# Kernel optimization log

Measured on AMD Instinct MI355X. Metric: run time of the kernel, lower is better.

The kernel has to match this reference:

```python
import jax, jax.numpy as jnp
import numpy as np

D_MODEL = 1024
NUM_HEADS = 16
D_HEAD = D_MODEL // NUM_HEADS


def setup_inputs() -> dict:
    key = jax.random.key(0)
    ks = jax.random.split(key, 9)
    s = 1.0 / np.sqrt(D_MODEL)
    return {
        "x": jax.random.normal(ks[0], (2, 2048, D_MODEL), dtype=jnp.float32),
        "Wq": jax.random.normal(ks[1], (D_MODEL, D_MODEL), dtype=jnp.float32) * s,
        "bq": jnp.zeros((D_MODEL,), dtype=jnp.float32),
        "Wk": jax.random.normal(ks[2], (D_MODEL, D_MODEL), dtype=jnp.float32) * s,
        "bk": jnp.zeros((D_MODEL,), dtype=jnp.float32),
        "Wv": jax.random.normal(ks[3], (D_MODEL, D_MODEL), dtype=jnp.float32) * s,
        "bv": jnp.zeros((D_MODEL,), dtype=jnp.float32),
        "Wo": jax.random.normal(ks[4], (D_MODEL, D_MODEL), dtype=jnp.float32) * s,
        "bo": jnp.zeros((D_MODEL,), dtype=jnp.float32),
    }


def reference(x, Wq, bq, Wk, bk, Wv, bv, Wo, bo):
    B, S, D = x.shape
    H, Dh = NUM_HEADS, D_HEAD

    def split_heads(t):  # [B,S,D] -> [B,H,S,Dh]
        return t.reshape(B, S, H, Dh).transpose(0, 2, 1, 3)

    # Linear layers: y = x @ W^T + b (torch nn.Linear convention)
    Q = split_heads(x @ Wq.T + bq)
    K = split_heads(x @ Wk.T + bk)
    V = split_heads(x @ Wv.T + bv)

    scale = 1.0 / jnp.sqrt(jnp.asarray(Dh, dtype=x.dtype))
    scores = jnp.einsum("bhqd,bhkd->bhqk", Q, K) * scale  # [B,H,S,S]
    attn = jax.nn.softmax(scores, axis=-1)
    context = jnp.einsum("bhqk,bhkd->bhqd", attn, V)  # [B,H,S,Dh]
    context = context.transpose(0, 2, 1, 3).reshape(B, S, D)
    return context @ Wo.T + bo
```

## Files before the change

### kernel.cpp

```cpp
#include <hip/hip_runtime.h>


#define T_TOK 4096
#define DM    1024
#define SQ    2048
#define NH    16
#define DH    64

typedef unsigned short u16;
typedef unsigned int   u32;
typedef __bf16 bf16x8 __attribute__((ext_vector_type(8)));
typedef float  f32x4  __attribute__((ext_vector_type(4)));
typedef float  f32x16 __attribute__((ext_vector_type(16)));
typedef u32    u32x4  __attribute__((ext_vector_type(4)));

__device__ __forceinline__ u16 f2bf(float f) {
  u32 u = __builtin_bit_cast(u32, f);
  u32 r = (u + 0x7FFFu + ((u >> 16) & 1u)) >> 16;
  return (u16)r;
}

#if __has_builtin(__builtin_amdgcn_cvt_pk_bf16_f32)
typedef __bf16 bf16x2 __attribute__((ext_vector_type(2)));
__device__ __forceinline__ u32 pk2bf(float a, float b) {
  bf16x2 h = __builtin_amdgcn_cvt_pk_bf16_f32(a, b);
  return __builtin_bit_cast(u32, h);
}
#else
__device__ __forceinline__ u32 pk2bf(float a, float b) {
  u32 r;
  asm("v_cvt_pk_bf16_f32 %0, %1, %2" : "=v"(r) : "v"(a), "v"(b));
  return r;
}
#endif

__device__ __forceinline__ void gld16(const void* g, void* l) {
  __builtin_amdgcn_global_load_lds(
      (const __attribute__((address_space(1))) u32*)g,
      (__attribute__((address_space(3))) u32*)l, 16, 0, 0);
}

__global__ void cast_bf16_kernel(const float* __restrict__ x,
    const float* __restrict__ w0, const float* __restrict__ w1,
    const float* __restrict__ w2, const float* __restrict__ w3,
    u16* __restrict__ xb, u16* __restrict__ o0, u16* __restrict__ o1,
    u16* __restrict__ o2, u16* __restrict__ o3)
{
  const float* src; u16* dst; int n;
  switch (blockIdx.y) {
    case 0:  src = x;  dst = xb; n = T_TOK * DM; break;
    case 1:  src = w0; dst = o0; n = DM * DM; break;
    case 2:  src = w1; dst = o1; n = DM * DM; break;
    case 3:  src = w2; dst = o2; n = DM * DM; break;
    default: src = w3; dst = o3; n = DM * DM; break;
  }
  const int stride = gridDim.x * blockDim.x;
  for (int i = blockIdx.x * blockDim.x + threadIdx.x; i * 4 < n; i += stride) {
    float4 v = ((const float4*)src)[i];
    ushort4 o;
    o.x = f2bf(v.x); o.y = f2bf(v.y); o.z = f2bf(v.z); o.w = f2bf(v.w);
    ((ushort4*)dst)[i] = o;
  }
}

__device__ __forceinline__ void gemm_core_128x128(
    u16* lds, const u16* __restrict__ Ab, const u16* __restrict__ Bb,
    f32x4 acc[4][4])
{
  u16* As = lds;
  u16* Bs = lds + 8192;
  const int tid = threadIdx.x, lane = tid & 63, w = tid >> 6;
  const int waveM = w >> 1, waveN = w & 1;
  const int col = lane & 15, quad = lane >> 4;
  const int srow = lane >> 3;
  const int sg0  = (lane & 7) ^ srow;

  for (int k0 = 0; k0 < DM; k0 += 64) {
    #pragma unroll
    for (int i = 0; i < 4; ++i) {
      const int rb = w * 32 + i * 8;
      const int sg = sg0 ^ ((rb >> 3) & 3);
      gld16(Ab + (size_t)(rb + srow) * DM + k0 + sg * 8, &As[rb * 64]);
      gld16(Bb + (size_t)(rb + srow) * DM + k0 + sg * 8, &Bs[rb * 64]);
    }
    __syncthreads();
    #pragma unroll
    for (int c = 0; c < 2; ++c) {
      bf16x8 af[4], bg[4];
      #pragma unroll
      for (int i = 0; i < 4; ++i) {
        const int row = waveM * 64 + i * 16 + col;
        const int gp = (c * 4 + quad) ^ (row & 7) ^ ((row >> 3) & 3);
        af[i] = *(const bf16x8*)&As[row * 64 + gp * 8];
      }
      #pragma unroll
      for (int j = 0; j < 4; ++j) {
        const int row = waveN * 64 + j * 16 + col;
        const int gp = (c * 4 + quad) ^ (row & 7) ^ ((row >> 3) & 3);
        bg[j] = *(const bf16x8*)&Bs[row * 64 + gp * 8];
      }
      #pragma unroll
      for (int i = 0; i < 4; ++i) {
        #pragma unroll
        for (int j = 0; j < 4; ++j)
          acc[i][j] = __builtin_amdgcn_mfma_f32_16x16x32_bf16(af[i], bg[j], acc[i][j], 0, 0, 0);
      }
    }
    __syncthreads();
  }
}

__device__ __forceinline__ void gemm_core_128x64(
    u16* lds, const u16* __restrict__ Ab, const u16* __restrict__ Bb,
    f32x4 acc[4][2])
{
  u16* As = lds;
  u16* Bs = lds + 8192;
  const int tid = threadIdx.x, lane = tid & 63, w = tid >> 6;
  const int waveM = w >> 1, waveN = w & 1;
  const int col = lane & 15, quad = lane >> 4;
  const int srow = lane >> 3;
  const int sg0  = (lane & 7) ^ srow;

  for (int k0 = 0; k0 < DM; k0 += 64) {
    #pragma unroll
    for (int i = 0; i < 4; ++i) {
      const int rb = w * 32 + i * 8;
      const int sg = sg0 ^ ((rb >> 3) & 3);
      gld16(Ab + (size_t)(rb + srow) * DM + k0 + sg * 8, &As[rb * 64]);
    }
    #pragma unroll
    for (int i = 0; i < 2; ++i) {
      const int rb = w * 16 + i * 8;
      const int sg = sg0 ^ ((rb >> 3) & 3);
      gld16(Bb + (size_t)(rb + srow) * DM + k0 + sg * 8, &Bs[rb * 64]);
    }
    __syncthreads();
    #pragma unroll
    for (int c = 0; c < 2; ++c) {
      bf16x8 af[4], bg[2];
      #pragma unroll
      for (int i = 0; i < 4; ++i) {
        const int row = waveM * 64 + i * 16 + col;
        const int gp = (c * 4 + quad) ^ (row & 7) ^ ((row >> 3) & 3);
        af[i] = *(const bf16x8*)&As[row * 64 + gp * 8];
      }
      #pragma unroll
      for (int j = 0; j < 2; ++j) {
        const int row = waveN * 32 + j * 16 + col;
        const int gp = (c * 4 + quad) ^ (row & 7) ^ ((row >> 3) & 3);
        bg[j] = *(const bf16x8*)&Bs[row * 64 + gp * 8];
      }
      #pragma unroll
      for (int i = 0; i < 4; ++i) {
        #pragma unroll
        for (int j = 0; j < 2; ++j)
          acc[i][j] = __builtin_amdgcn_mfma_f32_16x16x32_bf16(af[i], bg[j], acc[i][j], 0, 0, 0);
      }
    }
    __syncthreads();
  }
}

__global__ __launch_bounds__(256) void gemm_qkv_kernel(
    const u16* __restrict__ xb,
    const u16* __restrict__ Wqb, const u16* __restrict__ Wkb, const u16* __restrict__ Wvb,
    const float* __restrict__ bq, const float* __restrict__ bk, const float* __restrict__ bv,
    u16* __restrict__ Qs, u16* __restrict__ Kh, u16* __restrict__ Vt)
{
  __shared__ __align__(16) u16 smem[128 * 136];
  u16* tr = smem;
  const int z = blockIdx.z;
  const u16*   Wb   = (z == 0) ? Wqb : (z == 1) ? Wkb : Wvb;
  const float* bias = (z == 0) ? bq  : (z == 1) ? bk  : bv;
  const float scale = (z == 0) ? 0.18033688011112042f : 1.0f;

  const int tid = threadIdx.x;
  const int lane = tid & 63, w = tid >> 6;
  const int waveM = w >> 1, waveN = w & 1;
  const int col = lane & 15, quad = lane >> 4;
  const f32x4 zf = {0.f, 0.f, 0.f, 0.f};

  if (z == 2) {
    if (blockIdx.y >= 32) return;
    f32x4 acc[4][4];
    #pragma unroll
    for (int i = 0; i < 4; ++i) {
      #pragma unroll
      for (int j = 0; j < 4; ++j) acc[i][j] = zf;
    }
    gemm_core_128x128(smem, xb + (size_t)(blockIdx.y * 128) * DM,
                      Wb + (size_t)(blockIdx.x * 128) * DM, acc);
    #pragma unroll
    for (int j = 0; j < 4; ++j) {
      const int cl = waveN * 64 + j * 16 + col;
      const float bb = bias[blockIdx.x * 128 + cl];
      #pragma unroll
      for (int i = 0; i < 4; ++i) {
        const int tl = waveM * 64 + i * 16 + quad * 4;
        ushort4 pk;
        pk.x = f2bf(acc[i][j][0] + bb); pk.y = f2bf(acc[i][j][1] + bb);
        pk.z = f2bf(acc[i][j][2] + bb); pk.w = f2bf(acc[i][j][3] + bb);
        *(ushort4*)&tr[cl * 136 + tl] = pk;
      }
    }
    __syncthreads();
    const int t0 = blockIdx.y * 128;
    const int b = t0 >> 11, sBase = t0 & 2047;
    #pragma unroll
    for (int rep = 0; rep < 8; ++rep) {
      const int chunk = rep * 256 + tid;
      const int row = chunk >> 4, off = (chunk & 15) * 8;
      const int c = blockIdx.x * 128 + row;
      const int h = c >> 6, d = c & 63;
      uint4 v = *(const uint4*)&tr[row * 136 + off];
      *(uint4*)&Vt[((size_t)(b * NH + h) * DH + d) * SQ + sBase + off] = v;
    }
  } else {
    f32x4 acc[4][2];
    #pragma unroll
    for (int i = 0; i < 4; ++i) {
      #pragma unroll
      for (int j = 0; j < 2; ++j) acc[i][j] = zf;
    }
    gemm_core_128x64(smem, Wb + (size_t)(blockIdx.x * 128) * DM,
                     xb + (size_t)(blockIdx.y * 64) * DM, acc);
    u16* out = (z == 0) ? Qs : Kh;
    const int chBase  = blockIdx.x * 128 + waveM * 64;
    const int tokBase = blockIdx.y * 64 + waveN * 32;
    #pragma unroll
    for (int i = 0; i < 4; ++i) {
      const int c0 = chBase + i * 16 + quad * 4;
      const int hh = c0 >> 6, d0 = c0 & 63;
      const float4 bb = *(const float4*)&bias[c0];
      #pragma unroll
      for (int j = 0; j < 2; ++j) {
        const int t = tokBase + j * 16 + col;
        const int b = t >> 11, s = t & 2047;
        ushort4 pk;
        pk.x = f2bf((acc[i][j][0] + bb.x) * scale);
        pk.y = f2bf((acc[i][j][1] + bb.y) * scale);
        pk.z = f2bf((acc[i][j][2] + bb.z) * scale);
        pk.w = f2bf((acc[i][j][3] + bb.w) * scale);
        *(ushort4*)&out[((size_t)(b * NH + hh) * SQ + s) * DH + d0] = pk;
      }
    }
  }
}

__global__ __launch_bounds__(256, 2) void attn_kernel(
    const u16* __restrict__ Qs, const u16* __restrict__ Kh,
    const u16* __restrict__ Vt, u16* __restrict__ ctx)
{
  __shared__ __align__(16) char smem[64 * 1024];
  u16* KtB = (u16*)smem;
  u16* VlB = (u16*)(smem + 32768);
  f32x4* red  = (f32x4*)smem;
  float* lred = (float*)(smem + 32768);

  const int tid = threadIdx.x, lane = tid & 63, w = tid >> 6;
  const int l31 = lane & 31, h = lane >> 5;
  const int bh = blockIdx.y, q0 = blockIdx.x * 64;
  const u16* Qb = Qs + ((size_t)bh * SQ + q0) * DH;
  const u16* Kb = Kh + (size_t)bh * SQ * DH;
  const u16* Vb = Vt + (size_t)bh * DH * SQ;

  bf16x8 qreg[2][4];
  #pragma unroll
  for (int qt = 0; qt < 2; ++qt) {
    #pragma unroll
    for (int ks = 0; ks < 4; ++ks)
      qreg[qt][ks] = *(const bf16x8*)(Qb + (size_t)(qt * 32 + l31) * DH
                                         + ks * 16 + h * 8);
  }

  #pragma unroll
  for (int i = 0; i < 4; ++i) {
    const int rb = w * 32 + i * 8;
    const int rowloc = rb + (lane >> 3);
    const int sg = (lane & 7) ^ (lane >> 3) ^ ((rb >> 3) & 3);
    gld16(Kb + (size_t)rowloc * DH + sg * 8, &KtB[rb * 64]);
  }
  #pragma unroll
  for (int i = 0; i < 4; ++i) {
    const int rb = w * 16 + i * 4;
    const int rowloc = rb + (lane >> 4);
    const int sg = (lane & 15) ^ (rowloc & 15);
    gld16(Vb + (size_t)rowloc * SQ + sg * 8, &VlB[rb * 128]);
  }

  f32x16 cacc[2][2];
  #pragma unroll
  for (int dt = 0; dt < 2; ++dt)
    #pragma unroll
    for (int qt = 0; qt < 2; ++qt)
      #pragma unroll
      for (int e = 0; e < 16; ++e) cacc[dt][qt][e] = 0.f;
  float l_s[2] = {0.f, 0.f};
  __syncthreads();

  for (int kt = 0; kt < SQ / 128; ++kt) {
    const int cur = kt & 1;
    u16* Kt = KtB + cur * 8192;
    u16* Vl = VlB + cur * 8192;
    if (kt + 1 < SQ / 128) {
      const int nxt = cur ^ 1, s1 = (kt + 1) * 128;
      u16* Ktn = KtB + nxt * 8192;
      u16* Vln = VlB + nxt * 8192;
      #pragma unroll
      for (int i = 0; i < 4; ++i) {
        const int rb = w * 32 + i * 8;
        const int rowloc = rb + (lane >> 3);
        const int sg = (lane & 7) ^ (lane >> 3) ^ ((rb >> 3) & 3);
        gld16(Kb + (size_t)(s1 + rowloc) * DH + sg * 8, &Ktn[rb * 64]);
      }
      #pragma unroll
      for (int i = 0; i < 4; ++i) {
        const int rb = w * 16 + i * 4;
        const int rowloc = rb + (lane >> 4);
        const int sg = (lane & 15) ^ (rowloc & 15);
        gld16(Vb + (size_t)rowloc * SQ + s1 + sg * 8, &Vln[rb * 128]);
      }
    }

    f32x16 sacc[2];
    #pragma unroll
    for (int qt = 0; qt < 2; ++qt)
      #pragma unroll
      for (int e = 0; e < 16; ++e) sacc[qt][e] = 0.f;
    #pragma unroll
    for (int ks = 0; ks < 4; ++ks) {
      const int row = w * 32 + l31;
      const int gp = (2 * ks + h) ^ (l31 & 7) ^ ((l31 >> 3) & 3);
      bf16x8 kf = *(const bf16x8*)&Kt[row * 64 + gp * 8];
      sacc[0] = __builtin_amdgcn_mfma_f32_32x32x16_bf16(kf, qreg[0][ks], sacc[0], 0, 0, 0);
      sacc[1] = __builtin_amdgcn_mfma_f32_32x32x16_bf16(kf, qreg[1][ks], sacc[1], 0, 0, 0);
    }

    u32 Pp[2][4][2];
    #pragma unroll
    for (int qt = 0; qt < 2; ++qt) {
      float p[16];
      #pragma unroll
      for (int e = 0; e < 16; ++e)
        p[e] = __builtin_amdgcn_exp2f(sacc[qt][e]);
      float t0 = (p[0] + p[1]) + (p[2] + p[3]);
      float t1 = (p[4] + p[5]) + (p[6] + p[7]);
      float t2 = (p[8] + p[9]) + (p[10] + p[11]);
      float t3 = (p[12] + p[13]) + (p[14] + p[15]);
      l_s[qt] += (t0 + t1) + (t2 + t3);
      #pragma unroll
      for (int rg = 0; rg < 4; ++rg) {
        Pp[qt][rg][0] = pk2bf(p[4 * rg + 0], p[4 * rg + 1]);
        Pp[qt][rg][1] = pk2bf(p[4 * rg + 2], p[4 * rg + 3]);
      }
    }

    #pragma unroll
    for (int ks = 0; ks < 2; ++ks) {
      bf16x8 pf[2];
      #pragma unroll
      for (int qt = 0; qt < 2; ++qt) {
        u32 own0 = h ? Pp[qt][2 * ks + 1][0] : Pp[qt][2 * ks][0];
        u32 own1 = h ? Pp[qt][2 * ks + 1][1] : Pp[qt][2 * ks][1];
        u32 snd0 = h ? Pp[qt][2 * ks][0] : Pp[qt][2 * ks + 1][0];
        u32 snd1 = h ? Pp[qt][2 * ks][1] : Pp[qt][2 * ks + 1][1];
        u32 rcv0 = (u32)__shfl_xor((int)snd0, 32, 64);
        u32 rcv1 = (u32)__shfl_xor((int)snd1, 32, 64);
        u32x4 fw;
        fw.x = h ? rcv0 : own0;
        fw.y = h ? rcv1 : own1;
        fw.z = h ? own0 : rcv0;
        fw.w = h ? own1 : rcv1;
        pf[qt] = __builtin_bit_cast(bf16x8, fw);
      }
      #pragma unroll
      for (int dt = 0; dt < 2; ++dt) {
        const int row = dt * 32 + l31;
        const int gp = (4 * w + 2 * ks + h) ^ (row & 15);
        bf16x8 vf = *(const bf16x8*)&Vl[row * 128 + gp * 8];
        cacc[dt][0] = __builtin_amdgcn_mfma_f32_32x32x16_bf16(vf, pf[0], cacc[dt][0], 0, 0, 0);
        cacc[dt][1] = __builtin_amdgcn_mfma_f32_32x32x16_bf16(vf, pf[1], cacc[dt][1], 0, 0, 0);
      }
    }
    __syncthreads();
  }

  float lq[2];
  #pragma unroll
  for (int qt = 0; qt < 2; ++qt) {
    lq[qt] = l_s[qt] + __shfl_xor(l_s[qt], 32, 64);
    if (h == 0) lred[(w * 2 + qt) * 32 + l31] = lq[qt];
  }
  const int b = bh >> 4, hd = bh & 15;
  #pragma unroll
  for (int qt = 0; qt < 2; ++qt) {
    __syncthreads();
    #pragma unroll
    for (int dt = 0; dt < 2; ++dt) {
      #pragma unroll
      for (int c = 0; c < 4; ++c) {
        f32x4 ch;
        ch[0] = cacc[dt][qt][4 * c + 0]; ch[1] = cacc[dt][qt][4 * c + 1];
        ch[2] = cacc[dt][qt][4 * c + 2]; ch[3] = cacc[dt][qt][4 * c + 3];
        red[((w * 2 + dt) * 4 + c) * 64 + lane] = ch;
      }
    }
    __syncthreads();
    const int dt = w >> 1, c0 = (w & 1) * 2;
    f32x4 sum[2];
    #pragma unroll
    for (int j = 0; j < 2; ++j) { sum[j][0]=0; sum[j][1]=0; sum[j][2]=0; sum[j][3]=0; }
    #pragma unroll
    for (int sw = 0; sw < 4; ++sw) {
      #pragma unroll
      for (int j = 0; j < 2; ++j)
        sum[j] += red[((sw * 2 + dt) * 4 + c0 + j) * 64 + lane];
    }
    float lsum = lred[(0 * 2 + qt) * 32 + l31] + lred[(1 * 2 + qt) * 32 + l31]
               + lred[(2 * 2 + qt) * 32 + l31] + lred[(3 * 2 + qt) * 32 + l31];
    const float inv = 1.0f / lsum;
    const int s = q0 + qt * 32 + l31;
    #pragma unroll
    for (int j = 0; j < 2; ++j) {
      const int d0 = dt * 32 + (c0 + j) * 8 + 4 * h;
      ushort4 pk;
      pk.x = f2bf(sum[j][0] * inv); pk.y = f2bf(sum[j][1] * inv);
      pk.z = f2bf(sum[j][2] * inv); pk.w = f2bf(sum[j][3] * inv);
      *(ushort4*)&ctx[(size_t)(b * SQ + s) * DM + hd * DH + d0] = pk;
    }
  }
}

__global__ __launch_bounds__(256) void gemm_out_kernel(
    const u16* __restrict__ ctx, const u16* __restrict__ Wob,
    const float* __restrict__ bo, float* __restrict__ out)
{
  __shared__ __align__(16) u16 As[64 * 64];
  __shared__ __align__(16) u16 Bs[64 * 64];
  const u16* Ab = ctx + (size_t)(blockIdx.y * 64) * DM;
  const u16* Bb = Wob + (size_t)(blockIdx.x * 64) * DM;
  const int tid = threadIdx.x, lane = tid & 63, w = tid >> 6;
  const int waveM = w >> 1, waveN = w & 1;
  const int col = lane & 15, quad = lane >> 4;
  const int srow = lane >> 3;
  const int sg0  = (lane & 7) ^ srow;

  f32x4 acc[2][2];
  const f32x4 zf = {0.f, 0.f, 0.f, 0.f};
  #pragma unroll
  for (int i = 0; i < 2; ++i) {
    #pragma unroll
    for (int j = 0; j < 2; ++j) acc[i][j] = zf;
  }

  for (int k0 = 0; k0 < DM; k0 += 64) {
    #pragma unroll
    for (int i = 0; i < 2; ++i) {
      const int rb = w * 16 + i * 8;
      const int sg = sg0 ^ ((rb >> 3) & 3);
      gld16(Ab + (size_t)(rb + srow) * DM + k0 + sg * 8, &As[rb * 64]);
      gld16(Bb + (size_t)(rb + srow) * DM + k0 + sg * 8, &Bs[rb * 64]);
    }
    __syncthreads();
    #pragma unroll
    for (int c = 0; c < 2; ++c) {
      bf16x8 af[2], bg[2];
      #pragma unroll
      for (int i = 0; i < 2; ++i) {
        const int row = waveM * 32 + i * 16 + col;
        const int gp = (c * 4 + quad) ^ (row & 7) ^ ((row >> 3) & 3);
        af[i] = *(const bf16x8*)&As[row * 64 + gp * 8];
      }
      #pragma unroll
      for (int j = 0; j < 2; ++j) {
        const int row = waveN * 32 + j * 16 + col;
        const int gp = (c * 4 + quad) ^ (row & 7) ^ ((row >> 3) & 3);
        bg[j] = *(const bf16x8*)&Bs[row * 64 + gp * 8];
      }
      #pragma unroll
      for (int i = 0; i < 2; ++i) {
        #pragma unroll
        for (int j = 0; j < 2; ++j)
          acc[i][j] = __builtin_amdgcn_mfma_f32_16x16x32_bf16(af[i], bg[j], acc[i][j], 0, 0, 0);
      }
    }
    __syncthreads();
  }

  const int rowBase = blockIdx.y * 64 + waveM * 32;
  const int colBase = blockIdx.x * 64 + waveN * 32;
  #pragma unroll
  for (int j = 0; j < 2; ++j) {
    const int c = colBase + j * 16 + col;
    const float bb = bo[c];
    #pragma unroll
    for (int i = 0; i < 2; ++i) {
      #pragma unroll
      for (int r = 0; r < 4; ++r) {
        const int t = rowBase + i * 16 + quad * 4 + r;
        out[(size_t)t * DM + c] = acc[i][j][r] + bb;
      }
    }
  }
}

extern "C" void kernel_launch(void* const* d_in, const int* in_sizes, int n_in,
                              void* d_out, int out_size, void* d_ws, size_t ws_size,
                              hipStream_t stream) {
  const float* x  = (const float*)d_in[0];
  const float* Wq = (const float*)d_in[1];
  const float* bq = (const float*)d_in[2];
  const float* Wk = (const float*)d_in[3];
  const float* bk = (const float*)d_in[4];
  const float* Wv = (const float*)d_in[5];
  const float* bv = (const float*)d_in[6];
  const float* Wo = (const float*)d_in[7];
  const float* bo = (const float*)d_in[8];

  char* ws = (char*)d_ws;
  u16* xb  = (u16*)(ws);
  u16* Wqb = (u16*)(ws + (8ull  << 20));
  u16* Wkb = (u16*)(ws + (10ull << 20));
  u16* Wvb = (u16*)(ws + (12ull << 20));
  u16* Wob = (u16*)(ws + (14ull << 20));
  u16* Qs  = (u16*)(ws + (16ull << 20));
  u16* Kh  = (u16*)(ws + (24ull << 20));
  u16* Vt  = (u16*)(ws + (32ull << 20));
  u16* ctx = xb;

  cast_bf16_kernel<<<dim3(256, 5), 256, 0, stream>>>(x, Wq, Wk, Wv, Wo,
                                                     xb, Wqb, Wkb, Wvb, Wob);
  gemm_qkv_kernel<<<dim3(8, 64, 3), 256, 0, stream>>>(xb, Wqb, Wkb, Wvb,
                                                      bq, bk, bv, Qs, Kh, Vt);
  attn_kernel<<<dim3(32, 32), 256, 0, stream>>>(Qs, Kh, Vt, ctx);
  gemm_out_kernel<<<dim3(16, 64), 256, 0, stream>>>(ctx, Wob, bo, (float*)d_out);
  (void)in_sizes; (void)n_in; (void)out_size; (void)ws_size;
}
```

Before: 207.6 us.

## Shrink attention KV tile to 64 and split waves by query/key halves

The attention kernel now streams 64-key tiles instead of 128-key tiles. Each wave owns one 32-query tile and one 32-key sub-tile rather than two query tiles, which halves the accumulator and score registers per wave. LDS drops from 64KB to 33KB and launch bounds rise to 4 blocks per CU, aiming for higher occupancy and better latency hiding. The cost is twice as many loop iterations and barriers, and a different cross-wave reduction layout at the end.

```diff
diff --git a/kernel.cpp b/kernel.cpp
--- a/kernel.cpp
+++ b/kernel.cpp
@@ -248,187 +248,145 @@
   }
 }
 
-__global__ __launch_bounds__(256, 2) void attn_kernel(
+__global__ __launch_bounds__(256, 4) void attn_kernel(
     const u16* __restrict__ Qs, const u16* __restrict__ Kh,
     const u16* __restrict__ Vt, u16* __restrict__ ctx)
 {
-  __shared__ __align__(16) char smem[64 * 1024];
+  __shared__ __align__(16) char smem[33 * 1024];
   u16* KtB = (u16*)smem;
-  u16* VlB = (u16*)(smem + 32768);
+  u16* VlB = (u16*)(smem + 16384);
   f32x4* red  = (f32x4*)smem;
   float* lred = (float*)(smem + 32768);
 
   const int tid = threadIdx.x, lane = tid & 63, w = tid >> 6;
   const int l31 = lane & 31, h = lane >> 5;
+  const int qt = w & 1, st = w >> 1;
   const int bh = blockIdx.y, q0 = blockIdx.x * 64;
   const u16* Qb = Qs + ((size_t)bh * SQ + q0) * DH;
   const u16* Kb = Kh + (size_t)bh * SQ * DH;
   const u16* Vb = Vt + (size_t)bh * DH * SQ;
-
-  bf16x8 qreg[2][4];
-  #pragma unroll
-  for (int qt = 0; qt < 2; ++qt) {
-    #pragma unroll
-    for (int ks = 0; ks < 4; ++ks)
-      qreg[qt][ks] = *(const bf16x8*)(Qb + (size_t)(qt * 32 + l31) * DH
-                                         + ks * 16 + h * 8);
-  }
-
-  #pragma unroll
-  for (int i = 0; i < 4; ++i) {
-    const int rb = w * 32 + i * 8;
-    const int rowloc = rb + (lane >> 3);
-    const int sg = (lane & 7) ^ (lane >> 3) ^ ((rb >> 3) & 3);
-    gld16(Kb + (size_t)rowloc * DH + sg * 8, &KtB[rb * 64]);
-  }
-  #pragma unroll
-  for (int i = 0; i < 4; ++i) {
-    const int rb = w * 16 + i * 4;
-    const int rowloc = rb + (lane >> 4);
-    const int sg = (lane & 15) ^ (rowloc & 15);
-    gld16(Vb + (size_t)rowloc * SQ + sg * 8, &VlB[rb * 128]);
-  }
-
-  f32x16 cacc[2][2];
+  const int srow = lane >> 3;
+  const int sgl  = (lane & 7) ^ srow;
+
+  bf16x8 qreg[4];
+  #pragma unroll
+  for (int ks = 0; ks < 4; ++ks)
+    qreg[ks] = *(const bf16x8*)(Qb + (size_t)(qt * 32 + l31) * DH + ks * 16 + h * 8);
+
+  #pragma unroll
+  for (int i = 0; i < 2; ++i) {
+    const int rb = w * 16 + i * 8;
+    const int sg = sgl ^ ((rb >> 3) & 3);
+    gld16(Kb + (size_t)(rb + srow) * DH + sg * 8, &KtB[rb * 64]);
+    gld16(Vb + (size_t)(rb + srow) * SQ + sg * 8, &VlB[rb * 64]);
+  }
+
+  f32x16 cacc[2];
   #pragma unroll
   for (int dt = 0; dt < 2; ++dt)
     #pragma unroll
-    for (int qt = 0; qt < 2; ++qt)
-      #pragma unroll
-      for (int e = 0; e < 16; ++e) cacc[dt][qt][e] = 0.f;
-  float l_s[2] = {0.f, 0.f};
+    for (int e = 0; e < 16; ++e) cacc[dt][e] = 0.f;
+  float l_s = 0.f;
   __syncthreads();
 
-  for (int kt = 0; kt < SQ / 128; ++kt) {
+  for (int kt = 0; kt < SQ / 64; ++kt) {
     const int cur = kt & 1;
-    u16* Kt = KtB + cur * 8192;
-    u16* Vl = VlB + cur * 8192;
-    if (kt + 1 < SQ / 128) {
-      const int nxt = cur ^ 1, s1 = (kt + 1) * 128;
-      u16* Ktn = KtB + nxt * 8192;
-      u16* Vln = VlB + nxt * 8192;
-      #pragma unroll
-      for (int i = 0; i < 4; ++i) {
-        const int rb = w * 32 + i * 8;
-        const int rowloc = rb + (lane >> 3);
-        const int sg = (lane & 7) ^ (lane >> 3) ^ ((rb >> 3) & 3);
-        gld16(Kb + (size_t)(s1 + rowloc) * DH + sg * 8, &Ktn[rb * 64]);
-      }
-      #pragma unroll
-      for (int i = 0; i < 4; ++i) {
-        const int rb = w * 16 + i * 4;
-        const int rowloc = rb + (lane >> 4);
-        const int sg = (lane & 15) ^ (rowloc & 15);
-        gld16(Vb + (size_t)rowloc * SQ + s1 + sg * 8, &Vln[rb * 128]);
-      }
-    }
-
-    f32x16 sacc[2];
-    #pragma unroll
-    for (int qt = 0; qt < 2; ++qt)
-      #pragma unroll
-      for (int e = 0; e < 16; ++e) sacc[qt][e] = 0.f;
+    u16* Kt = KtB + cur * 4096;
+    u16* Vl = VlB + cur * 4096;
+    if (kt + 1 < SQ / 64) {
+      const int nxt = cur ^ 1, s1 = (kt + 1) * 64;
+      u16* Ktn = KtB + nxt * 4096;
+      u16* Vln = VlB + nxt * 4096;
+      #pragma unroll
+      for (int i = 0; i < 2; ++i) {
+        const int rb = w * 16 + i * 8;
+        const int sg = sgl ^ ((rb >> 3) & 3);
+        gld16(Kb + (size_t)(s1 + rb + srow) * DH + sg * 8, &Ktn[rb * 64]);
+        gld16(Vb + (size_t)(rb + srow) * SQ + s1 + sg * 8, &Vln[rb * 64]);
+      }
+    }
+
+    f32x16 sacc;
+    #pragma unroll
+    for (int e = 0; e < 16; ++e) sacc[e] = 0.f;
     #pragma unroll
     for (int ks = 0; ks < 4; ++ks) {
-      const int row = w * 32 + l31;
+      const int row = st * 32 + l31;
       const int gp = (2 * ks + h) ^ (l31 & 7) ^ ((l31 >> 3) & 3);
       bf16x8 kf = *(const bf16x8*)&Kt[row * 64 + gp * 8];
-      sacc[0] = __builtin_amdgcn_mfma_f32_32x32x16_bf16(kf, qreg[0][ks], sacc[0], 0, 0, 0);
-      sacc[1] = __builtin_amdgcn_mfma_f32_32x32x16_bf16(kf, qreg[1][ks], sacc[1], 0, 0, 0);
-    }
-
-    u32 Pp[2][4][2];
-    #pragma unroll
-    for (int qt = 0; qt < 2; ++qt) {
+      sacc = __builtin_amdgcn_mfma_f32_32x32x16_bf16(kf, qreg[ks], sacc, 0, 0, 0);
+    }
+
+    u32 Pp[4][2];
+    {
       float p[16];
       #pragma unroll
       for (int e = 0; e < 16; ++e)
-        p[e] = __builtin_amdgcn_exp2f(sacc[qt][e]);
+        p[e] = __builtin_amdgcn_exp2f(sacc[e]);
       float t0 = (p[0] + p[1]) + (p[2] + p[3]);
       float t1 = (p[4] + p[5]) + (p[6] + p[7]);
       float t2 = (p[8] + p[9]) + (p[10] + p[11]);
       float t3 = (p[12] + p[13]) + (p[14] + p[15]);
-      l_s[qt] += (t0 + t1) + (t2 + t3);
+      l_s += (t0 + t1) + (t2 + t3);
       #pragma unroll
       for (int rg = 0; rg < 4; ++rg) {
-        Pp[qt][rg][0] = pk2bf(p[4 * rg + 0], p[4 * rg + 1]);
-        Pp[qt][rg][1] = pk2bf(p[4 * rg + 2], p[4 * rg + 3]);
+        Pp[rg][0] = pk2bf(p[4 * rg + 0], p[4 * rg + 1]);
+        Pp[rg][1] = pk2bf(p[4 * rg + 2], p[4 * rg + 3]);
       }
     }
 
     #pragma unroll
     for (int ks = 0; ks < 2; ++ks) {
-      bf16x8 pf[2];
-      #pragma unroll
-      for (int qt = 0; qt < 2; ++qt) {
-        u32 own0 = h ? Pp[qt][2 * ks + 1][0] : Pp[qt][2 * ks][0];
-        u32 own1 = h ? Pp[qt][2 * ks + 1][1] : Pp[qt][2 * ks][1];
-        u32 snd0 = h ? Pp[qt][2 * ks][0] : Pp[qt][2 * ks + 1][0];
-        u32 snd1 = h ? Pp[qt][2 * ks][1] : Pp[qt][2 * ks + 1][1];
-        u32 rcv0 = (u32)__shfl_xor((int)snd0, 32, 64);
-        u32 rcv1 = (u32)__shfl_xor((int)snd1, 32, 64);
-        u32x4 fw;
-        fw.x = h ? rcv0 : own0;
-        fw.y = h ? rcv1 : own1;
-        fw.z = h ? own0 : rcv0;
-        fw.w = h ? own1 : rcv1;
-        pf[qt] = __builtin_bit_cast(bf16x8, fw);
-      }
+      u32 own0 = h ? Pp[2 * ks + 1][0] : Pp[2 * ks][0];
+      u32 own1 = h ? Pp[2 * ks + 1][1] : Pp[2 * ks][1];
+      u32 snd0 = h ? Pp[2 * ks][0] : Pp[2 * ks + 1][0];
+      u32 snd1 = h ? Pp[2 * ks][1] : Pp[2 * ks + 1][1];
+      u32 rcv0 = (u32)__shfl_xor((int)snd0, 32, 64);
+      u32 rcv1 = (u32)__shfl_xor((int)snd1, 32, 64);
+      u32x4 fw;
+      fw.x = h ? rcv0 : own0;
+      fw.y = h ? rcv1 : own1;
+      fw.z = h ? own0 : rcv0;
+      fw.w = h ? own1 : rcv1;
+      bf16x8 pf = __builtin_bit_cast(bf16x8, fw);
       #pragma unroll
       for (int dt = 0; dt < 2; ++dt) {
         const int row = dt * 32 + l31;
-        const int gp = (4 * w + 2 * ks + h) ^ (row & 15);
-        bf16x8 vf = *(const bf16x8*)&Vl[row * 128 + gp * 8];
-        cacc[dt][0] = __builtin_amdgcn_mfma_f32_32x32x16_bf16(vf, pf[0], cacc[dt][0], 0, 0, 0);
-        cacc[dt][1] = __builtin_amdgcn_mfma_f32_32x32x16_bf16(vf, pf[1], cacc[dt][1], 0, 0, 0);
-      }
-    }
-    __syncthreads();
-  }
-
-  float lq[2];
-  #pragma unroll
-  for (int qt = 0; qt < 2; ++qt) {
-    lq[qt] = l_s[qt] + __shfl_xor(l_s[qt], 32, 64);
-    if (h == 0) lred[(w * 2 + qt) * 32 + l31] = lq[qt];
-  }
+        const int gp = (4 * st + 2 * ks + h) ^ (l31 & 7) ^ ((l31 >> 3) & 3);
+        bf16x8 vf = *(const bf16x8*)&Vl[row * 64 + gp * 8];
+        cacc[dt] = __builtin_amdgcn_mfma_f32_32x32x16_bf16(vf, pf, cacc[dt], 0, 0, 0);
+      }
+    }
+    __syncthreads();
+  }
+
+  float lq = l_s + __shfl_xor(l_s, 32, 64);
+  if (h == 0) lred[w * 32 + l31] = lq;
+  #pragma unroll
+  for (int dt = 0; dt < 2; ++dt) {
+    #pragma unroll
+    for (int c = 0; c < 4; ++c) {
+      f32x4 ch;
+      ch[0] = cacc[dt][4 * c + 0]; ch[1] = cacc[dt][4 * c + 1];
+      ch[2] = cacc[dt][4 * c + 2]; ch[3] = cacc[dt][4 * c + 3];
+      red[((w * 2 + dt) * 4 + c) * 64 + lane] = ch;
+    }
+  }
+  __syncthreads();
+  const int qt2 = w & 1, dt2 = w >> 1;
   const int b = bh >> 4, hd = bh & 15;
-  #pragma unroll
-  for (int qt = 0; qt < 2; ++qt) {
-    __syncthreads();
-    #pragma unroll
-    for (int dt = 0; dt < 2; ++dt) {
-      #pragma unroll
-      for (int c = 0; c < 4; ++c) {
-        f32x4 ch;
-        ch[0] = cacc[dt][qt][4 * c + 0]; ch[1] = cacc[dt][qt][4 * c + 1];
-        ch[2] = cacc[dt][qt][4 * c + 2]; ch[3] = cacc[dt][qt][4 * c + 3];
-        red[((w * 2 + dt) * 4 + c) * 64 + lane] = ch;
-      }
-    }
-    __syncthreads();
-    const int dt = w >> 1, c0 = (w & 1) * 2;
-    f32x4 sum[2];
-    #pragma unroll
-    for (int j = 0; j < 2; ++j) { sum[j][0]=0; sum[j][1]=0; sum[j][2]=0; sum[j][3]=0; }
-    #pragma unroll
-    for (int sw = 0; sw < 4; ++sw) {
-      #pragma unroll
-      for (int j = 0; j < 2; ++j)
-        sum[j] += red[((sw * 2 + dt) * 4 + c0 + j) * 64 + lane];
-    }
-    float lsum = lred[(0 * 2 + qt) * 32 + l31] + lred[(1 * 2 + qt) * 32 + l31]
-               + lred[(2 * 2 + qt) * 32 + l31] + lred[(3 * 2 + qt) * 32 + l31];
-    const float inv = 1.0f / lsum;
-    const int s = q0 + qt * 32 + l31;
-    #pragma unroll
-    for (int j = 0; j < 2; ++j) {
-      const int d0 = dt * 32 + (c0 + j) * 8 + 4 * h;
-      ushort4 pk;
-      pk.x = f2bf(sum[j][0] * inv); pk.y = f2bf(sum[j][1] * inv);
-      pk.z = f2bf(sum[j][2] * inv); pk.w = f2bf(sum[j][3] * inv);
-      *(ushort4*)&ctx[(size_t)(b * SQ + s) * DM + hd * DH + d0] = pk;
-    }
+  const float lsum = lred[qt2 * 32 + l31] + lred[(2 + qt2) * 32 + l31];
+  const float inv = 1.0f / lsum;
+  const int s = q0 + qt2 * 32 + l31;
+  #pragma unroll
+  for (int c = 0; c < 4; ++c) {
+    f32x4 sum = red[((qt2 * 2 + dt2) * 4 + c) * 64 + lane];
+    sum += red[(((2 + qt2) * 2 + dt2) * 4 + c) * 64 + lane];
+    const int d0 = dt2 * 32 + c * 8 + 4 * h;
+    ushort4 pk;
+    pk.x = f2bf(sum[0] * inv); pk.y = f2bf(sum[1] * inv);
+    pk.z = f2bf(sum[2] * inv); pk.w = f2bf(sum[3] * inv);
+    *(ushort4*)&ctx[(size_t)(b * SQ + s) * DM + hd * DH + d0] = pk;
   }
 }
 
```

After: 205.4 us. No clear change (-1.0%).
